# Kernel tuning notes

Measured on AMD Instinct MI355X. Metric: run time of the kernel, lower is better.

Reference implementation:

```python
import jax, jax.numpy as jnp
import numpy as np

B, N, CIN, CD, NE = 64, 256, 768, 32, 8192

def setup_inputs() -> dict:
    key = jax.random.key(0)
    ks = jax.random.split(key, 8)
    z = jax.random.normal(ks[0], (B, N, CIN), dtype=jnp.float32)
    # Embedding weight: trunc_normal_(mean=0, std=1, a=-3, b=3)
    emb_weight = jax.random.truncated_normal(ks[1], -3.0, 3.0, (NE, CD)).astype(jnp.float32)
    # Linears stored as [in, out] so y = x @ W + b
    W_compress = jax.random.normal(ks[2], (CIN, CD), dtype=jnp.float32) / np.sqrt(CIN)
    b_compress = jnp.zeros((CD,), dtype=jnp.float32)
    W_ct = jax.random.normal(ks[3], (CD, CD), dtype=jnp.float32) / np.sqrt(CD)
    b_ct = jnp.zeros((CD,), dtype=jnp.float32)
    W_expand = jax.random.normal(ks[4], (CD, CIN), dtype=jnp.float32) / np.sqrt(CD)
    b_expand = jnp.zeros((CIN,), dtype=jnp.float32)
    return {"z": z, "emb_weight": emb_weight, "W_compress": W_compress,
            "b_compress": b_compress, "W_ct": W_ct, "b_ct": b_ct,
            "W_expand": W_expand, "b_expand": b_expand}

def reference(z, emb_weight, W_compress, b_compress, W_ct, b_ct, W_expand, b_expand):
    sg = jax.lax.stop_gradient
    # torch uses embedding.weight.data -> detached codebook input
    implicit_codebook = sg(emb_weight) @ W_ct + b_ct              # [NE, CD]
    zc = z @ W_compress + b_compress                              # [B, N, CD]
    z_flat = zc.reshape(-1, zc.shape[-1])                         # [B*N, CD]
    # squared distance: ||z||^2 + ||c||^2 - 2 z.c
    d = (jnp.sum(z_flat ** 2, axis=1, keepdims=True)
         + jnp.sum(implicit_codebook ** 2, axis=1)
         - 2.0 * jnp.einsum('bd,nd->bn', z_flat, implicit_codebook))  # [B*N, NE]
    indices = jnp.argmin(d, axis=1)                               # [B*N]
    z_q = implicit_codebook[indices]                              # [B*N, CD]
    # training-path losses (codebook + 2.0 * commitment)
    loss = (jnp.mean((sg(z_q) - z_flat) ** 2)
            + 2.0 * jnp.mean((z_q - sg(z_flat)) ** 2))
    # straight-through estimator
    z_st = sg(z_q) + z_flat - sg(z_flat)
    out = z_st.reshape(zc.shape) @ W_expand + b_expand            # [B, N, CIN]
    return out, loss
```

## Files before the change

kernel.cpp:

```cpp
#include <hip/hip_runtime.h>

constexpr int CIN = 768;
constexpr int CD  = 32;
constexpr int NE  = 8192;
constexpr int M   = 16384;
constexpr int SCH = 64;
constexpr int CPC = NE / SCH;
constexpr int PTB = 128;
#define MARGIN 0.05f

typedef short short8 __attribute__((ext_vector_type(8)));
typedef float f32x4  __attribute__((ext_vector_type(4)));

__device__ inline void split_bf16(float x, unsigned short& h, unsigned short& l) {
  unsigned u = __float_as_uint(x);
  unsigned hb = (u + 0x7FFFu + ((u >> 16) & 1u)) >> 16;
  float hf = __uint_as_float(hb << 16);
  float r = x - hf;
  unsigned u2 = __float_as_uint(r);
  unsigned lb = (u2 + 0x7FFFu + ((u2 >> 16) & 1u)) >> 16;
  h = (unsigned short)hb;
  l = (unsigned short)lb;
}

__device__ inline void gload_lds16(const void* g, void* l) {
  __builtin_amdgcn_global_load_lds(
      (const __attribute__((address_space(1))) unsigned int*)g,
      (__attribute__((address_space(3))) unsigned int*)l, 16, 0, 0);
}

__global__ __launch_bounds__(256) void k_light(
    const float* __restrict__ emb, const float* __restrict__ Wct,
    const float* __restrict__ bct, const float* __restrict__ Wc,
    const float* __restrict__ We,
    float* __restrict__ cb, float* __restrict__ cnorm,
    unsigned short* __restrict__ ch, unsigned short* __restrict__ cl,
    unsigned short* __restrict__ WeTh, unsigned short* __restrict__ WeTl,
    unsigned short* __restrict__ WcTh, unsigned short* __restrict__ WcTl) {
  __shared__ float smem[CD * CD];
  const int t = threadIdx.x;
  if (blockIdx.x < 1024) {
    for (int i = t; i < CD * CD; i += 256) smem[i] = Wct[i];
    __syncthreads();
    const int g   = blockIdx.x * 256 + t;
    const int row = g >> 5;
    const int col = g & 31;
    float acc = bct[col];
    const float* er = emb + row * CD;
    #pragma unroll
    for (int k = 0; k < CD; ++k) acc = fmaf(er[k], smem[k * CD + col], acc);
    cb[g] = acc;
    unsigned short h, l;
    split_bf16(acc, h, l);
    ch[g] = h; cl[g] = l;
    float v = acc * acc;
    #pragma unroll
    for (int m = 16; m >= 1; m >>= 1) v += __shfl_xor(v, m, 64);
    if (col == 0) cnorm[row] = v;
    return;
  }
  if (blockIdx.x < 1027) {
    const int n = (blockIdx.x - 1024) * 256 + t;
    #pragma unroll
    for (int k = 0; k < CD; ++k) {
      unsigned short h, l;
      split_bf16(We[(long)k * CIN + n], h, l);
      WeTh[n * CD + k] = h;
      WeTl[n * CD + k] = l;
    }
    return;
  }
  {
    const int n  = t >> 3;
    const int k0 = (t & 7) * 96;
    for (int k = k0; k < k0 + 96; ++k) {
      unsigned short h, l;
      split_bf16(Wc[k * CD + n], h, l);
      WcTh[n * CIN + k] = h;
      WcTl[n * CIN + k] = l;
    }
  }
}

__global__ __launch_bounds__(256) void k_compress(
    const float* __restrict__ z,
    const unsigned short* __restrict__ WcTh, const unsigned short* __restrict__ WcTl,
    const float* __restrict__ bc,
    float* __restrict__ zc, unsigned short* __restrict__ zh,
    unsigned short* __restrict__ zl) {
  __shared__ float ps[3 * 544];
  const int t    = threadIdx.x;
  const int lane = t & 63;
  const int wv   = t >> 6;
  const int n    = lane & 15;
  const int quad = lane >> 4;
  const int r0   = blockIdx.x * 16;

  const float* za = z + (long)(r0 + n) * CIN + wv * 192 + quad * 8;
  const unsigned short* bh0 = WcTh + n * CIN + wv * 192 + quad * 8;
  const unsigned short* bl0 = WcTl + n * CIN + wv * 192 + quad * 8;
  const unsigned short* bh1 = bh0 + 16 * CIN;
  const unsigned short* bl1 = bl0 + 16 * CIN;

  f32x4 acc0, acc1;
  if (wv == 0) {
    const float b0 = bc[n];
    const float b1 = bc[n + 16];
    acc0 = (f32x4){b0, b0, b0, b0};
    acc1 = (f32x4){b1, b1, b1, b1};
  } else {
    acc0 = (f32x4){0.f, 0.f, 0.f, 0.f};
    acc1 = (f32x4){0.f, 0.f, 0.f, 0.f};
  }

  #pragma unroll
  for (int kt = 0; kt < 6; ++kt) {
    const float4 za0 = *(const float4*)(za + kt * 32);
    const float4 za1 = *(const float4*)(za + kt * 32 + 4);
    short8 Ah, Al;
    {
      unsigned short h, l;
      split_bf16(za0.x, h, l); Ah[0] = (short)h; Al[0] = (short)l;
      split_bf16(za0.y, h, l); Ah[1] = (short)h; Al[1] = (short)l;
      split_bf16(za0.z, h, l); Ah[2] = (short)h; Al[2] = (short)l;
      split_bf16(za0.w, h, l); Ah[3] = (short)h; Al[3] = (short)l;
      split_bf16(za1.x, h, l); Ah[4] = (short)h; Al[4] = (short)l;
      split_bf16(za1.y, h, l); Ah[5] = (short)h; Al[5] = (short)l;
      split_bf16(za1.z, h, l); Ah[6] = (short)h; Al[6] = (short)l;
      split_bf16(za1.w, h, l); Ah[7] = (short)h; Al[7] = (short)l;
    }
    const short8 Bh0 = *(const short8*)(bh0 + kt * 32);
    const short8 Bl0 = *(const short8*)(bl0 + kt * 32);
    const short8 Bh1 = *(const short8*)(bh1 + kt * 32);
    const short8 Bl1 = *(const short8*)(bl1 + kt * 32);
    acc0 = __builtin_amdgcn_mfma_f32_16x16x32_bf16(Ah, Bh0, acc0, 0, 0, 0);
    acc0 = __builtin_amdgcn_mfma_f32_16x16x32_bf16(Ah, Bl0, acc0, 0, 0, 0);
    acc0 = __builtin_amdgcn_mfma_f32_16x16x32_bf16(Al, Bh0, acc0, 0, 0, 0);
    acc1 = __builtin_amdgcn_mfma_f32_16x16x32_bf16(Ah, Bh1, acc1, 0, 0, 0);
    acc1 = __builtin_amdgcn_mfma_f32_16x16x32_bf16(Ah, Bl1, acc1, 0, 0, 0);
    acc1 = __builtin_amdgcn_mfma_f32_16x16x32_bf16(Al, Bh1, acc1, 0, 0, 0);
  }

  if (wv != 0) {
    float* pp = ps + (wv - 1) * 544;
    #pragma unroll
    for (int r = 0; r < 4; ++r) {
      const int row = quad * 4 + r;
      pp[row * 17 + n]       = acc0[r];
      pp[272 + row * 17 + n] = acc1[r];
    }
  }
  __syncthreads();
  if (wv == 0) {
    #pragma unroll
    for (int r = 0; r < 4; ++r) {
      const int row = quad * 4 + r;
      const float v0 = ((acc0[r] + ps[row * 17 + n]) + ps[544 + row * 17 + n])
                       + ps[1088 + row * 17 + n];
      const float v1 = ((acc1[r] + ps[272 + row * 17 + n]) + ps[816 + row * 17 + n])
                       + ps[1360 + row * 17 + n];
      const long i0 = (long)(r0 + row) * CD + n;
      zc[i0]      = v0;
      zc[i0 + 16] = v1;
      unsigned short h, l;
      split_bf16(-2.f * v0, h, l); zh[i0] = h;      zl[i0] = l;
      split_bf16(-2.f * v1, h, l); zh[i0 + 16] = h; zl[i0 + 16] = l;
    }
  }
}

__global__ __launch_bounds__(256) void k_argmin(
    const unsigned short* __restrict__ zh, const unsigned short* __restrict__ zl,
    const unsigned short* __restrict__ ch, const unsigned short* __restrict__ cl,
    const float* __restrict__ cnorm,
    float* __restrict__ pd) {
  __shared__ __align__(16) unsigned short chs[CPC * CD];
  __shared__ __align__(16) unsigned short cls[CPC * CD];
  const int pb   = blockIdx.x & (M / PTB - 1);
  const int cid  = blockIdx.x >> 7;
  const int lane = threadIdx.x & 63;
  const int wv   = threadIdx.x >> 6;
  const int col  = lane & 15;
  const int quad = lane >> 4;
  const int p0   = pb * PTB + wv * 32;

  const char* chg = (const char*)ch + (long)cid * (CPC * CD * 2);
  const char* clg = (const char*)cl + (long)cid * (CPC * CD * 2);
  #pragma unroll
  for (int s = 0; s < 2; ++s) {
    const int lo = s * 4096 + wv * 1024;
    gload_lds16(chg + lo + lane * 16, (char*)chs + lo);
    gload_lds16(clg + lo + lane * 16, (char*)cls + lo);
  }

  const short8 Ah0 = *(const short8*)(zh + (long)(p0 + col) * CD + quad * 8);
  const short8 Al0 = *(const short8*)(zl + (long)(p0 + col) * CD + quad * 8);
  const short8 Ah1 = *(const short8*)(zh + (long)(p0 + 16 + col) * CD + quad * 8);
  const short8 Al1 = *(const short8*)(zl + (long)(p0 + 16 + col) * CD + quad * 8);

  const int jb = cid * CPC;
  float cnv[8];
  #pragma unroll
  for (int tt = 0; tt < 8; ++tt) cnv[tt] = cnorm[jb + tt * 16 + col];

  float bd0[4], bd1[4];
  #pragma unroll
  for (int r = 0; r < 4; ++r) { bd0[r] = 1e30f; bd1[r] = 1e30f; }

  __syncthreads();

  #pragma unroll
  for (int tt = 0; tt < 8; ++tt) {
    const short8 Bh = *(const short8*)(chs + (tt * 16 + col) * CD + quad * 8);
    const short8 Bl = *(const short8*)(cls + (tt * 16 + col) * CD + quad * 8);
    const f32x4 c4 = {cnv[tt], cnv[tt], cnv[tt], cnv[tt]};
    f32x4 g0 = __builtin_amdgcn_mfma_f32_16x16x32_bf16(Ah0, Bh, c4, 0, 0, 0);
    g0 = __builtin_amdgcn_mfma_f32_16x16x32_bf16(Ah0, Bl, g0, 0, 0, 0);
    g0 = __builtin_amdgcn_mfma_f32_16x16x32_bf16(Al0, Bh, g0, 0, 0, 0);
    f32x4 g1 = __builtin_amdgcn_mfma_f32_16x16x32_bf16(Ah1, Bh, c4, 0, 0, 0);
    g1 = __builtin_amdgcn_mfma_f32_16x16x32_bf16(Ah1, Bl, g1, 0, 0, 0);
    g1 = __builtin_amdgcn_mfma_f32_16x16x32_bf16(Al1, Bh, g1, 0, 0, 0);
    #pragma unroll
    for (int r = 0; r < 4; ++r) {
      bd0[r] = fminf(bd0[r], g0[r]);
      bd1[r] = fminf(bd1[r], g1[r]);
    }
  }

  #pragma unroll
  for (int mm = 1; mm <= 8; mm <<= 1) {
    #pragma unroll
    for (int r = 0; r < 4; ++r) {
      bd0[r] = fminf(bd0[r], __shfl_xor(bd0[r], mm, 64));
      bd1[r] = fminf(bd1[r], __shfl_xor(bd1[r], mm, 64));
    }
  }
  if (col == 0) {
    #pragma unroll
    for (int r = 0; r < 4; ++r) {
      const int pA = p0 + quad * 4 + r;
      pd[(long)pA * SCH + cid] = bd0[r];
      const int pB = pA + 16;
      pd[(long)pB * SCH + cid] = bd1[r];
    }
  }
}

__global__ __launch_bounds__(256) void k_rescue(
    const float* __restrict__ zc, const float* __restrict__ cb,
    const float* __restrict__ cnorm,
    const float* __restrict__ pd,
    float* __restrict__ zq, unsigned short* __restrict__ zqh,
    unsigned short* __restrict__ zql, float* __restrict__ lpart) {
  const int lane = threadIdx.x & 63;
  const int wv   = threadIdx.x >> 6;
  const int p    = blockIdx.x * 4 + wv;

  const float m = pd[(long)p * SCH + lane];
  float dstar = m;
  #pragma unroll
  for (int mm = 1; mm <= 32; mm <<= 1) dstar = fminf(dstar, __shfl_xor(dstar, mm, 64));
  unsigned long long mask = __ballot(m <= dstar + MARGIN);

  float zr[CD];
  {
    const float4* z4 = (const float4*)(zc + (long)p * CD);
    #pragma unroll
    for (int q = 0; q < 8; ++q) {
      float4 v = z4[q];
      zr[4 * q + 0] = v.x; zr[4 * q + 1] = v.y; zr[4 * q + 2] = v.z; zr[4 * q + 3] = v.w;
    }
  }

  float bd = 1e30f;
  int   bj = 0x7fffffff;
  while (mask) {
    const int c = (int)__builtin_ctzll(mask);
    mask &= mask - 1;
    #pragma unroll
    for (int u = 0; u < 2; ++u) {
      const int j = c * CPC + u * 64 + lane;
      const float4* crow = (const float4*)(cb + (long)j * CD);
      float acc = 0.f;
      #pragma unroll
      for (int q = 0; q < 8; ++q) {
        float4 cv = crow[q];
        acc = fmaf(zr[4 * q + 0], cv.x, acc);
        acc = fmaf(zr[4 * q + 1], cv.y, acc);
        acc = fmaf(zr[4 * q + 2], cv.z, acc);
        acc = fmaf(zr[4 * q + 3], cv.w, acc);
      }
      const float d = fmaf(-2.f, acc, cnorm[j]);
      if (d < bd) { bd = d; bj = j; }
    }
  }
  #pragma unroll
  for (int mm = 1; mm <= 32; mm <<= 1) {
    const float od = __shfl_xor(bd, mm, 64);
    const int   oj = __shfl_xor(bj, mm, 64);
    if (od < bd || (od == bd && oj < bj)) { bd = od; bj = oj; }
  }

  float ls = 0.f;
  if (lane < 32) {
    const float cv = cb[(long)bj * CD + lane];
    const float zv = zc[(long)p * CD + lane];
    zq[(long)p * CD + lane] = cv;
    unsigned short hh, ll;
    split_bf16(cv, hh, ll);
    zqh[(long)p * CD + lane] = hh;
    zql[(long)p * CD + lane] = ll;
    const float df = cv - zv;
    ls = df * df;
  }
  #pragma unroll
  for (int mm = 1; mm <= 32; mm <<= 1) ls += __shfl_xor(ls, mm, 64);
  if (lane == 0) lpart[p] = ls;
}

__global__ __launch_bounds__(256) void k_expand(
    const unsigned short* __restrict__ zqh, const unsigned short* __restrict__ zql,
    const unsigned short* __restrict__ WeTh, const unsigned short* __restrict__ WeTl,
    const float* __restrict__ be,
    const float* __restrict__ lpart,
    float* __restrict__ out,
    float* __restrict__ out_loss) {
  __shared__ double redd[4];
  const int t = threadIdx.x;
  if (blockIdx.x == 1024) {
    double v = 0.0;
    for (int k = t; k < M; k += 256) v += (double)lpart[k];
    #pragma unroll
    for (int mm = 1; mm <= 32; mm <<= 1) v += __shfl_xor(v, mm, 64);
    if ((t & 63) == 0) redd[t >> 6] = v;
    __syncthreads();
    if (t == 0)
      out_loss[0] = (float)(3.0 * (redd[0] + redd[1] + redd[2] + redd[3]) / (double)(M * CD));
    return;
  }
  const int lane = t & 63;
  const int wv   = t >> 6;
  const int col  = lane & 15;
  const int quad = lane >> 4;
  const int r0   = blockIdx.x * 16;

  const short8 Ah = *(const short8*)(zqh + (long)(r0 + col) * CD + quad * 8);
  const short8 Al = *(const short8*)(zql + (long)(r0 + col) * CD + quad * 8);

  #pragma unroll
  for (int tt = 0; tt < 12; ++tt) {
    const int n0 = (wv * 12 + tt) * 16;
    const short8 Bh = *(const short8*)(WeTh + (long)(n0 + col) * CD + quad * 8);
    const short8 Bl = *(const short8*)(WeTl + (long)(n0 + col) * CD + quad * 8);
    const float bv = be[n0 + col];
    const f32x4 c4 = {bv, bv, bv, bv};
    f32x4 g = __builtin_amdgcn_mfma_f32_16x16x32_bf16(Ah, Bh, c4, 0, 0, 0);
    g = __builtin_amdgcn_mfma_f32_16x16x32_bf16(Ah, Bl, g, 0, 0, 0);
    g = __builtin_amdgcn_mfma_f32_16x16x32_bf16(Al, Bh, g, 0, 0, 0);
    #pragma unroll
    for (int r = 0; r < 4; ++r)
      out[(long)(r0 + quad * 4 + r) * CIN + n0 + col] = g[r];
  }
}

extern "C" void kernel_launch(void* const* d_in, const int* in_sizes, int n_in,
                              void* d_out, int out_size, void* d_ws, size_t ws_size,
                              hipStream_t stream) {
  const float* z   = (const float*)d_in[0];
  const float* emb = (const float*)d_in[1];
  const float* Wc  = (const float*)d_in[2];
  const float* bc  = (const float*)d_in[3];
  const float* Wct = (const float*)d_in[4];
  const float* bct = (const float*)d_in[5];
  const float* We  = (const float*)d_in[6];
  const float* be  = (const float*)d_in[7];
  float* out = (float*)d_out;

  float* cb    = (float*)d_ws;
  float* cnorm = cb + NE * CD;
  float* zc    = cnorm + NE;
  float* zq    = zc + M * CD;
  float* pd    = zq + M * CD;
  float* lpart = pd + (long)M * SCH;
  unsigned short* zh   = (unsigned short*)(lpart + M);
  unsigned short* zl   = zh + M * CD;
  unsigned short* ch   = zl + M * CD;
  unsigned short* cl   = ch + NE * CD;
  unsigned short* zqh  = cl + NE * CD;
  unsigned short* zql  = zqh + M * CD;
  unsigned short* WeTh = zql + M * CD;
  unsigned short* WeTl = WeTh + CIN * CD;
  unsigned short* WcTh = WeTl + CIN * CD;
  unsigned short* WcTl = WcTh + CIN * CD;

  k_light<<<1028, 256, 0, stream>>>(emb, Wct, bct, Wc, We,
                                    cb, cnorm, ch, cl, WeTh, WeTl, WcTh, WcTl);
  k_compress<<<M / 16, 256, 0, stream>>>(z, WcTh, WcTl, bc, zc, zh, zl);
  k_argmin<<<(M / PTB) * SCH, 256, 0, stream>>>(zh, zl, ch, cl, cnorm, pd);
  k_rescue<<<M / 4, 256, 0, stream>>>(zc, cb, cnorm, pd, zq, zqh, zql, lpart);
  k_expand<<<1024 + 1, 256, 0, stream>>>(zqh, zql, WeTh, WeTl, be, lpart,
                                         out, out + (long)M * CIN);
}
```

Measured before the change: 233.0 us.

## Split weight prep into parallel kernel, merge codebook into compress, transpose codebook for rescue

Weight bf16 splitting moves into a small fully parallel kernel (one element per thread) instead of a few serial-loop blocks. The codebook transform is merged into the compress kernel as extra blocks, so the two run concurrently in one launch. The codebook is also written transposed, so the rescue kernel reads coalesced float2 columns with each lane scoring two adjacent codes. This costs an extra kernel launch and an extra codebook copy in the workspace.

```diff
diff --git a/kernel.cpp b/kernel.cpp
--- a/kernel.cpp
+++ b/kernel.cpp
@@ -29,20 +29,44 @@
       (__attribute__((address_space(3))) unsigned int*)l, 16, 0, 0);
 }
 
-__global__ __launch_bounds__(256) void k_light(
+__global__ __launch_bounds__(256) void k_split(
+    const float* __restrict__ Wc, const float* __restrict__ We,
+    unsigned short* __restrict__ WcTh, unsigned short* __restrict__ WcTl,
+    unsigned short* __restrict__ WeTh, unsigned short* __restrict__ WeTl) {
+  const int t = threadIdx.x;
+  if (blockIdx.x < 96) {
+    const int idx = blockIdx.x * 256 + t;
+    const int k = idx >> 5, n = idx & 31;
+    unsigned short h, l;
+    split_bf16(Wc[idx], h, l);
+    WcTh[n * CIN + k] = h;
+    WcTl[n * CIN + k] = l;
+  } else {
+    const int idx = (blockIdx.x - 96) * 256 + t;
+    const int k = idx / CIN, n = idx - k * CIN;
+    unsigned short h, l;
+    split_bf16(We[idx], h, l);
+    WeTh[n * CD + k] = h;
+    WeTl[n * CD + k] = l;
+  }
+}
+
+__global__ __launch_bounds__(256) void k_main(
+    const float* __restrict__ z,
+    const unsigned short* __restrict__ WcTh, const unsigned short* __restrict__ WcTl,
+    const float* __restrict__ bc,
     const float* __restrict__ emb, const float* __restrict__ Wct,
-    const float* __restrict__ bct, const float* __restrict__ Wc,
-    const float* __restrict__ We,
-    float* __restrict__ cb, float* __restrict__ cnorm,
-    unsigned short* __restrict__ ch, unsigned short* __restrict__ cl,
-    unsigned short* __restrict__ WeTh, unsigned short* __restrict__ WeTl,
-    unsigned short* __restrict__ WcTh, unsigned short* __restrict__ WcTl) {
-  __shared__ float smem[CD * CD];
+    const float* __restrict__ bct,
+    float* __restrict__ zc, unsigned short* __restrict__ zh,
+    unsigned short* __restrict__ zl,
+    float* __restrict__ cb, float* __restrict__ cbT, float* __restrict__ cnorm,
+    unsigned short* __restrict__ ch, unsigned short* __restrict__ cl) {
+  __shared__ float smem[1632];
   const int t = threadIdx.x;
-  if (blockIdx.x < 1024) {
+  if (blockIdx.x >= 1024) {
     for (int i = t; i < CD * CD; i += 256) smem[i] = Wct[i];
     __syncthreads();
-    const int g   = blockIdx.x * 256 + t;
+    const int g   = (blockIdx.x - 1024) * 256 + t;
     const int row = g >> 5;
     const int col = g & 31;
     float acc = bct[col];
@@ -50,6 +74,7 @@
     #pragma unroll
     for (int k = 0; k < CD; ++k) acc = fmaf(er[k], smem[k * CD + col], acc);
     cb[g] = acc;
+    cbT[(long)col * NE + row] = acc;
     unsigned short h, l;
     split_bf16(acc, h, l);
     ch[g] = h; cl[g] = l;
@@ -59,37 +84,7 @@
     if (col == 0) cnorm[row] = v;
     return;
   }
-  if (blockIdx.x < 1027) {
-    const int n = (blockIdx.x - 1024) * 256 + t;
-    #pragma unroll
-    for (int k = 0; k < CD; ++k) {
-      unsigned short h, l;
-      split_bf16(We[(long)k * CIN + n], h, l);
-      WeTh[n * CD + k] = h;
-      WeTl[n * CD + k] = l;
-    }
-    return;
-  }
-  {
-    const int n  = t >> 3;
-    const int k0 = (t & 7) * 96;
-    for (int k = k0; k < k0 + 96; ++k) {
-      unsigned short h, l;
-      split_bf16(Wc[k * CD + n], h, l);
-      WcTh[n * CIN + k] = h;
-      WcTl[n * CIN + k] = l;
-    }
-  }
-}
-
-__global__ __launch_bounds__(256) void k_compress(
-    const float* __restrict__ z,
-    const unsigned short* __restrict__ WcTh, const unsigned short* __restrict__ WcTl,
-    const float* __restrict__ bc,
-    float* __restrict__ zc, unsigned short* __restrict__ zh,
-    unsigned short* __restrict__ zl) {
-  __shared__ float ps[3 * 544];
-  const int t    = threadIdx.x;
+  float* ps = smem;
   const int lane = t & 63;
   const int wv   = t >> 6;
   const int n    = lane & 15;
@@ -248,7 +243,7 @@
 
 __global__ __launch_bounds__(256) void k_rescue(
     const float* __restrict__ zc, const float* __restrict__ cb,
-    const float* __restrict__ cnorm,
+    const float* __restrict__ cbT, const float* __restrict__ cnorm,
     const float* __restrict__ pd,
     float* __restrict__ zq, unsigned short* __restrict__ zqh,
     unsigned short* __restrict__ zql, float* __restrict__ lpart) {
@@ -277,22 +272,20 @@
   while (mask) {
     const int c = (int)__builtin_ctzll(mask);
     mask &= mask - 1;
-    #pragma unroll
-    for (int u = 0; u < 2; ++u) {
-      const int j = c * CPC + u * 64 + lane;
-      const float4* crow = (const float4*)(cb + (long)j * CD);
-      float acc = 0.f;
-      #pragma unroll
-      for (int q = 0; q < 8; ++q) {
-        float4 cv = crow[q];
-        acc = fmaf(zr[4 * q + 0], cv.x, acc);
-        acc = fmaf(zr[4 * q + 1], cv.y, acc);
-        acc = fmaf(zr[4 * q + 2], cv.z, acc);
-        acc = fmaf(zr[4 * q + 3], cv.w, acc);
-      }
-      const float d = fmaf(-2.f, acc, cnorm[j]);
-      if (d < bd) { bd = d; bj = j; }
-    }
+    const int j0 = c * CPC + 2 * lane;
+    const float* cp = cbT + j0;
+    float acc0 = 0.f, acc1 = 0.f;
+    #pragma unroll
+    for (int k = 0; k < CD; ++k) {
+      const float2 cv = *(const float2*)(cp + (long)k * NE);
+      acc0 = fmaf(zr[k], cv.x, acc0);
+      acc1 = fmaf(zr[k], cv.y, acc1);
+    }
+    const float2 cn = *(const float2*)(cnorm + j0);
+    const float d0 = fmaf(-2.f, acc0, cn.x);
+    const float d1 = fmaf(-2.f, acc1, cn.y);
+    if (d0 < bd) { bd = d0; bj = j0; }
+    if (d1 < bd) { bd = d1; bj = j0 + 1; }
   }
   #pragma unroll
   for (int mm = 1; mm <= 32; mm <<= 1) {
@@ -392,12 +385,13 @@
   unsigned short* WeTl = WeTh + CIN * CD;
   unsigned short* WcTh = WeTl + CIN * CD;
   unsigned short* WcTl = WcTh + CIN * CD;
-
-  k_light<<<1028, 256, 0, stream>>>(emb, Wct, bct, Wc, We,
-                                    cb, cnorm, ch, cl, WeTh, WeTl, WcTh, WcTl);
-  k_compress<<<M / 16, 256, 0, stream>>>(z, WcTh, WcTl, bc, zc, zh, zl);
+  float* cbT = (float*)(WcTl + CIN * CD);
+
+  k_split<<<192, 256, 0, stream>>>(Wc, We, WcTh, WcTl, WeTh, WeTl);
+  k_main<<<2048, 256, 0, stream>>>(z, WcTh, WcTl, bc, emb, Wct, bct,
+                                   zc, zh, zl, cb, cbT, cnorm, ch, cl);
   k_argmin<<<(M / PTB) * SCH, 256, 0, stream>>>(zh, zl, ch, cl, cnorm, pd);
-  k_rescue<<<M / 4, 256, 0, stream>>>(zc, cb, cnorm, pd, zq, zqh, zql, lpart);
+  k_rescue<<<M / 4, 256, 0, stream>>>(zc, cb, cbT, cnorm, pd, zq, zqh, zql, lpart);
   k_expand<<<1024 + 1, 256, 0, stream>>>(zqh, zql, WeTh, WeTl, be, lpart,
                                          out, out + (long)M * CIN);
 }
```

After: 202.5 us. 1.15x faster.
